# Kernel tuning notes

Measured on AMD Instinct MI355X. Metric: run time of the kernel, lower is better.

The kernel has to match this reference:

```python
import jax, jax.numpy as jnp
import numpy as np

N, NFEAT, NHID, NHID2 = 10000, 512, 256, 128


def setup_inputs() -> dict:
    key = jax.random.key(0)
    k1, k2, k3, k4 = jax.random.split(key, 4)
    x = jax.random.normal(k1, (N, NFEAT), dtype=jnp.float32)
    # sparse-ish row-normalized adjacency, stored dense (as the module's spmm operand)
    raw = jax.random.uniform(k2, (N, N), dtype=jnp.float32)
    adj = jnp.where(raw > 0.995, raw, 0.0)
    adj = adj / jnp.maximum(adj.sum(axis=1, keepdims=True), 1e-6)
    W1 = jax.random.normal(k3, (NFEAT, NHID), dtype=jnp.float32) / np.sqrt(NFEAT)
    b1 = jnp.zeros((NHID,), dtype=jnp.float32)
    W2 = jax.random.normal(k4, (NHID, NHID2), dtype=jnp.float32) / np.sqrt(NHID)
    b2 = jnp.zeros((NHID2,), dtype=jnp.float32)
    return {"x": x, "adj": adj, "W1": W1, "b1": b1, "W2": W2, "b2": b2}


def gcn_conv(x, adj, W, b):
    # standard Kipf GCNConv: adj @ (x @ W) + b
    return adj @ (x @ W) + b


def reference(x, adj, W1, b1, W2, b2):
    h = jax.nn.relu(gcn_conv(x, adj, W1, b1))
    # dropout is identity in inference mode (training=False)
    h = jax.nn.relu(gcn_conv(h, adj, W2, b2))
    return h
```

## Files before the change

### kernel.cpp

```cpp
#include <hip/hip_runtime.h>

#define N_NODES 10000
#define NFEAT   512
#define NHID    256
#define NHID2   128
#define CAP     128

typedef __attribute__((ext_vector_type(8))) short bf16x8;
typedef __attribute__((ext_vector_type(4))) float f32x4;

__device__ __forceinline__ ushort f2bf(float f){
  union { float f; unsigned u; } v; v.f = f;
  unsigned r = v.u + 0x7FFFu + ((v.u >> 16) & 1u);
  return (ushort)(r >> 16);
}
__device__ __forceinline__ float bf2f(ushort u){
  union { unsigned u; float f; } v; v.u = ((unsigned)u) << 16; return v.f;
}

__global__ void k_cvt_all(const float* __restrict__ x, const float* __restrict__ W1,
                          const float* __restrict__ W2, ushort* __restrict__ xb,
                          ushort* __restrict__ w1t, ushort* __restrict__ w2t){
  const int b = blockIdx.x, t = threadIdx.x;
  if (b < 5000){
    int i = (b * 256 + t) * 4;
    float4 q = *(const float4*)(x + i);
    ushort4 o; o.x = f2bf(q.x); o.y = f2bf(q.y); o.z = f2bf(q.z); o.w = f2bf(q.w);
    *(ushort4*)(xb + i) = o;
  } else if (b < 5512){
    int id = (b - 5000) * 256 + t;
    int n = id >> 9, k = id & 511;
    w1t[id] = f2bf(W1[k * NHID + n]);
  } else {
    int id = (b - 5512) * 256 + t;
    int n = id >> 8, k = id & 255;
    w2t[id] = f2bf(W2[k * NHID2 + n]);
  }
}

template<int WR, int WC, bool OUT_BF16>
__launch_bounds__(256)
__global__ void k_gemm_bf16(const ushort* __restrict__ A, const ushort* __restrict__ Bt,
                            void* __restrict__ Cv, int M, int N, int K){
  const int lane = threadIdx.x & 63;
  const int w    = threadIdx.x >> 6;
  const int wr   = w >> 1, wc = w & 1;
  const int r16  = lane & 15;
  const int kg   = lane >> 4;
  const int BM = 2 * WR * 16, BN = 2 * WC * 16;
  const int row0 = blockIdx.x * BM + wr * WR * 16;
  const int col0 = blockIdx.y * BN + wc * WC * 16;

  f32x4 acc[WR][WC];
  #pragma unroll
  for (int r = 0; r < WR; r++)
    #pragma unroll
    for (int c = 0; c < WC; c++)
      acc[r][c] = (f32x4){0.f, 0.f, 0.f, 0.f};

  for (int k0 = 0; k0 < K; k0 += 32){
    bf16x8 a[WR], b[WC];
    #pragma unroll
    for (int r = 0; r < WR; r++){
      int ar = row0 + r * 16 + r16;
      if (ar >= M) ar = M - 1;
      a[r] = *(const bf16x8*)(A + (size_t)ar * K + k0 + kg * 8);
    }
    #pragma unroll
    for (int c = 0; c < WC; c++){
      int bc = col0 + c * 16 + r16;
      b[c] = *(const bf16x8*)(Bt + (size_t)bc * K + k0 + kg * 8);
    }
    #pragma unroll
    for (int r = 0; r < WR; r++)
      #pragma unroll
      for (int c = 0; c < WC; c++)
        acc[r][c] = __builtin_amdgcn_mfma_f32_16x16x32_bf16(a[r], b[c], acc[r][c], 0, 0, 0);
  }

  #pragma unroll
  for (int r = 0; r < WR; r++)
    #pragma unroll
    for (int c = 0; c < WC; c++){
      int col = col0 + c * 16 + r16;
      #pragma unroll
      for (int i = 0; i < 4; i++){
        int row = row0 + r * 16 + kg * 4 + i;
        if (row < M){
          if (OUT_BF16) ((ushort*)Cv)[(size_t)row * N + col] = f2bf(acc[r][c][i]);
          else          ((float*) Cv)[(size_t)row * N + col] = acc[r][c][i];
        }
      }
    }
}

__launch_bounds__(256)
__global__ void k_spmm1(const float* __restrict__ adj, const ushort* __restrict__ xw1b,
                        const float* __restrict__ b1, ushort* __restrict__ Hb,
                        int* __restrict__ row_nnz, int* __restrict__ pj, float* __restrict__ pa){
  const int r = blockIdx.x;
  const int t = threadIdx.x;
  const float* row = adj + (size_t)r * N_NODES;

  __shared__ int   sc[256];
  __shared__ int   lj[CAP];
  __shared__ float la[CAP];

  float4 vals[10];
  #pragma unroll
  for (int v = 0; v < 9; v++)
    vals[v] = *(const float4*)(row + v * 1024 + t * 4);
  vals[9] = (float4){0.f, 0.f, 0.f, 0.f};
  if (t < 196) vals[9] = *(const float4*)(row + 9216 + t * 4);

  int cnt = 0;
  #pragma unroll
  for (int v = 0; v < 10; v++)
    cnt += (vals[v].x != 0.f) + (vals[v].y != 0.f) + (vals[v].z != 0.f) + (vals[v].w != 0.f);

  sc[t] = cnt; __syncthreads();
  for (int off = 1; off < 256; off <<= 1){
    int u = 0;
    if (t >= off) u = sc[t - off];
    __syncthreads();
    sc[t] += u;
    __syncthreads();
  }
  int pos   = sc[t] - cnt;
  int total = sc[255];

  #pragma unroll
  for (int v = 0; v < 10; v++){
    float q[4] = {vals[v].x, vals[v].y, vals[v].z, vals[v].w};
    #pragma unroll
    for (int e = 0; e < 4; e++){
      if (q[e] != 0.f && pos < CAP){
        int idx = v * 1024 + t * 4 + e;
        lj[pos] = idx; la[pos] = q[e];
        pj[(size_t)r * CAP + pos] = idx;
        pa[(size_t)r * CAP + pos] = q[e];
        pos++;
      }
    }
  }
  __syncthreads();

  int n = min(total, CAP);
  if (t == 0) row_nnz[r] = n;

  float acc = 0.f;
  for (int k = 0; k < n; k++)
    acc += la[k] * bf2f(xw1b[(size_t)lj[k] * NHID + t]);
  Hb[(size_t)r * NHID + t] = f2bf(fmaxf(acc + b1[t], 0.f));
}

__launch_bounds__(128)
__global__ void k_spmm2(const int* __restrict__ row_nnz, const int* __restrict__ pj,
                        const float* __restrict__ pa, const float* __restrict__ hw2,
                        const float* __restrict__ b2, float* __restrict__ out){
  const int r = blockIdx.x;
  const int t = threadIdx.x;
  __shared__ int   lj[CAP];
  __shared__ float la[CAP];
  const int n = row_nnz[r];
  for (int k = t; k < n; k += 128){
    lj[k] = pj[(size_t)r * CAP + k];
    la[k] = pa[(size_t)r * CAP + k];
  }
  __syncthreads();
  float acc = 0.f;
  for (int k = 0; k < n; k++)
    acc += la[k] * hw2[(size_t)lj[k] * NHID2 + t];
  out[(size_t)r * NHID2 + t] = fmaxf(acc + b2[t], 0.f);
}

extern "C" void kernel_launch(void* const* d_in, const int* in_sizes, int n_in,
                              void* d_out, int out_size, void* d_ws, size_t ws_size,
                              hipStream_t stream){
  const float* x   = (const float*)d_in[0];
  const float* adj = (const float*)d_in[1];
  const float* W1  = (const float*)d_in[2];
  const float* b1  = (const float*)d_in[3];
  const float* W2  = (const float*)d_in[4];
  const float* b2  = (const float*)d_in[5];
  float* out = (float*)d_out;
  char*  ws  = (char*)d_ws;

  ushort* xb   = (ushort*)(ws);
  ushort* w1t  = (ushort*)(ws + 10240000);
  ushort* w2t  = (ushort*)(ws + 10502144);
  ushort* xw1b = (ushort*)(ws + 10567680);
  ushort* Hb   = (ushort*)(ws + 15687680);
  float*  hw2  = (float*)(ws + 20807680);
  int*    nnz  = (int*)(ws + 25927680);
  int*    pj   = (int*)(ws + 25967680);
  float*  pa   = (float*)(ws + 31087680);

  k_cvt_all<<<5640, 256, 0, stream>>>(x, W1, W2, xb, w1t, w2t);

  k_gemm_bf16<2,2,true><<<dim3(157, 4), 256, 0, stream>>>(xb, w1t, xw1b, N_NODES, NHID, NFEAT);

  k_spmm1<<<N_NODES, 256, 0, stream>>>(adj, xw1b, b1, Hb, nnz, pj, pa);

  k_gemm_bf16<2,2,false><<<dim3(157, 2), 256, 0, stream>>>(Hb, w2t, hw2, N_NODES, NHID2, NHID);

  k_spmm2<<<N_NODES, 128, 0, stream>>>(nnz, pj, pa, hw2, b2, out);
}
```

Before: 161.7 us.

## Split neighbor gather across eight slots with vectorized loads and wave-shuffle scan

The block-wide Hillis-Steele scan in spmm1 is replaced by a wave shuffle scan plus a per-wave offset combine, which removes many barriers. Both SpMM kernels now split each row's neighbor list across 8 slots of 32 lanes. Each lane issues 16-byte vector loads and the slot partials are reduced through shared memory. Column indices and values are packed into one int2 array, and the first GEMM tile grows to WR=4. The aim is more memory-level parallelism and fewer barriers in the gather stage. The cost is extra shared memory and a reduction step.

```diff
diff --git a/kernel.cpp b/kernel.cpp
--- a/kernel.cpp
+++ b/kernel.cpp
@@ -97,14 +97,16 @@
 __launch_bounds__(256)
 __global__ void k_spmm1(const float* __restrict__ adj, const ushort* __restrict__ xw1b,
                         const float* __restrict__ b1, ushort* __restrict__ Hb,
-                        int* __restrict__ row_nnz, int* __restrict__ pj, float* __restrict__ pa){
+                        int* __restrict__ row_nnz, int2* __restrict__ pja){
   const int r = blockIdx.x;
   const int t = threadIdx.x;
+  const int lane = t & 63, w = t >> 6;
   const float* row = adj + (size_t)r * N_NODES;
 
-  __shared__ int   sc[256];
+  __shared__ int   swave[4];
   __shared__ int   lj[CAP];
   __shared__ float la[CAP];
+  __shared__ float part[8 * NHID];
 
   float4 vals[10];
   #pragma unroll
@@ -118,16 +120,22 @@
   for (int v = 0; v < 10; v++)
     cnt += (vals[v].x != 0.f) + (vals[v].y != 0.f) + (vals[v].z != 0.f) + (vals[v].w != 0.f);
 
-  sc[t] = cnt; __syncthreads();
-  for (int off = 1; off < 256; off <<= 1){
-    int u = 0;
-    if (t >= off) u = sc[t - off];
-    __syncthreads();
-    sc[t] += u;
-    __syncthreads();
-  }
-  int pos   = sc[t] - cnt;
-  int total = sc[255];
+  int incl = cnt;
+  #pragma unroll
+  for (int d = 1; d < 64; d <<= 1){
+    int u = __shfl_up(incl, d, 64);
+    if (lane >= d) incl += u;
+  }
+  if (lane == 63) swave[w] = incl;
+  __syncthreads();
+  int woff = 0, total = 0;
+  #pragma unroll
+  for (int i = 0; i < 4; i++){
+    int s = swave[i];
+    total += s;
+    if (i < w) woff += s;
+  }
+  int pos = woff + incl - cnt;
 
   #pragma unroll
   for (int v = 0; v < 10; v++){
@@ -137,41 +145,72 @@
       if (q[e] != 0.f && pos < CAP){
         int idx = v * 1024 + t * 4 + e;
         lj[pos] = idx; la[pos] = q[e];
-        pj[(size_t)r * CAP + pos] = idx;
-        pa[(size_t)r * CAP + pos] = q[e];
+        pja[(size_t)r * CAP + pos] = make_int2(idx, __float_as_int(q[e]));
         pos++;
       }
     }
   }
   __syncthreads();
-
-  int n = min(total, CAP);
+  const int n = min(total, CAP);
   if (t == 0) row_nnz[r] = n;
 
-  float acc = 0.f;
-  for (int k = 0; k < n; k++)
-    acc += la[k] * bf2f(xw1b[(size_t)lj[k] * NHID + t]);
-  Hb[(size_t)r * NHID + t] = f2bf(fmaxf(acc + b1[t], 0.f));
-}
-
-__launch_bounds__(128)
-__global__ void k_spmm2(const int* __restrict__ row_nnz, const int* __restrict__ pj,
-                        const float* __restrict__ pa, const float* __restrict__ hw2,
-                        const float* __restrict__ b2, float* __restrict__ out){
+  const int slot = w * 2 + (lane >> 5);
+  const int l32  = lane & 31;
+  float accv[8] = {0.f,0.f,0.f,0.f,0.f,0.f,0.f,0.f};
+  for (int k = slot; k < n; k += 8){
+    bf16x8 rv = *(const bf16x8*)(xw1b + (size_t)lj[k] * NHID + l32 * 8);
+    float a = la[k];
+    #pragma unroll
+    for (int j = 0; j < 8; j++)
+      accv[j] += a * bf2f((ushort)rv[j]);
+  }
+  #pragma unroll
+  for (int j = 0; j < 8; j++)
+    part[slot * NHID + l32 * 8 + j] = accv[j];
+  __syncthreads();
+
+  float s = 0.f;
+  #pragma unroll
+  for (int i = 0; i < 8; i++)
+    s += part[i * NHID + t];
+  Hb[(size_t)r * NHID + t] = f2bf(fmaxf(s + b1[t], 0.f));
+}
+
+__launch_bounds__(256)
+__global__ void k_spmm2(const int* __restrict__ row_nnz, const int2* __restrict__ pja,
+                        const float* __restrict__ hw2, const float* __restrict__ b2,
+                        float* __restrict__ out){
   const int r = blockIdx.x;
   const int t = threadIdx.x;
   __shared__ int   lj[CAP];
   __shared__ float la[CAP];
+  __shared__ float part[8 * NHID2];
   const int n = row_nnz[r];
-  for (int k = t; k < n; k += 128){
-    lj[k] = pj[(size_t)r * CAP + k];
-    la[k] = pa[(size_t)r * CAP + k];
-  }
-  __syncthreads();
-  float acc = 0.f;
-  for (int k = 0; k < n; k++)
-    acc += la[k] * hw2[(size_t)lj[k] * NHID2 + t];
-  out[(size_t)r * NHID2 + t] = fmaxf(acc + b2[t], 0.f);
+  if (t < n){
+    int2 p = pja[(size_t)r * CAP + t];
+    lj[t] = p.x; la[t] = __int_as_float(p.y);
+  }
+  __syncthreads();
+
+  const int lane = t & 63, w = t >> 6;
+  const int slot = w * 2 + (lane >> 5);
+  const int l32  = lane & 31;
+  float4 accv = (float4){0.f,0.f,0.f,0.f};
+  for (int k = slot; k < n; k += 8){
+    float4 rv = *(const float4*)(hw2 + (size_t)lj[k] * NHID2 + l32 * 4);
+    float a = la[k];
+    accv.x += a * rv.x; accv.y += a * rv.y; accv.z += a * rv.z; accv.w += a * rv.w;
+  }
+  *(float4*)(part + slot * NHID2 + l32 * 4) = accv;
+  __syncthreads();
+
+  if (t < NHID2){
+    float s = 0.f;
+    #pragma unroll
+    for (int i = 0; i < 8; i++)
+      s += part[i * NHID2 + t];
+    out[(size_t)r * NHID2 + t] = fmaxf(s + b2[t], 0.f);
+  }
 }
 
 extern "C" void kernel_launch(void* const* d_in, const int* in_sizes, int n_in,
@@ -193,16 +232,15 @@
   ushort* Hb   = (ushort*)(ws + 15687680);
   float*  hw2  = (float*)(ws + 20807680);
   int*    nnz  = (int*)(ws + 25927680);
-  int*    pj   = (int*)(ws + 25967680);
-  float*  pa   = (float*)(ws + 31087680);
+  int2*   pja  = (int2*)(ws + 25967680);
 
   k_cvt_all<<<5640, 256, 0, stream>>>(x, W1, W2, xb, w1t, w2t);
 
-  k_gemm_bf16<2,2,true><<<dim3(157, 4), 256, 0, stream>>>(xb, w1t, xw1b, N_NODES, NHID, NFEAT);
-
-  k_spmm1<<<N_NODES, 256, 0, stream>>>(adj, xw1b, b1, Hb, nnz, pj, pa);
+  k_gemm_bf16<4,2,true><<<dim3(79, 4), 256, 0, stream>>>(xb, w1t, xw1b, N_NODES, NHID, NFEAT);
+
+  k_spmm1<<<N_NODES, 256, 0, stream>>>(adj, xw1b, b1, Hb, nnz, pja);
 
   k_gemm_bf16<2,2,false><<<dim3(157, 2), 256, 0, stream>>>(Hb, w2t, hw2, N_NODES, NHID2, NHID);
 
-  k_spmm2<<<N_NODES, 128, 0, stream>>>(nnz, pj, pa, hw2, b2, out);
-}
+  k_spmm2<<<N_NODES, 256, 0, stream>>>(nnz, pja, hw2, b2, out);
+}
```

Result: faster. 157.1 us (-2.9%).
